# Optimization experiments

Hardware: AMD Instinct MI355X
Metric: run time of the kernel (lower is better)

## Reference

```python
import jax, jax.numpy as jnp
import numpy as np

B, N, E = 64, 512, 262144
D_EMB = 128   # 2 * embedding_dim
D_H = 128     # residue_emb_dim == iegmn_lay_hid_dim
L = 5         # iegmn_n_lays
X_INIT = 0.25 # residual mix toward original coords (IEGMN x_connection_init)


def silu(x):
    return x * jax.nn.sigmoid(x)


def _edges(k):
    # within-graph random edges: pick a graph, then a node inside it
    g = jax.random.randint(k, (E,), 0, B)
    n = jax.random.randint(jax.random.fold_in(k, 1), (E,), 0, N)
    return (g * N + n).astype(jnp.int32)


def setup_inputs() -> dict:
    key = jax.random.key(0)
    ks = jax.random.split(key, 16)
    Nt = B * N
    s = 0.05
    feat = jax.random.normal(ks[0], (Nt, D_EMB), jnp.float32)
    coords = jax.random.normal(ks[1], (Nt, 3), jnp.float32)
    c_valid = (jax.random.uniform(ks[2], (B, N)) > 0.3).astype(jnp.float32)
    c_valid = c_valid.at[:, 0].set(1.0)  # avoid empty graphs
    return {
        'feat': feat,
        'coords': coords,
        'c_valid': c_valid,
        'edge_src': _edges(ks[3]), 'edge_dst': _edges(ks[4]),
        'cross_src': _edges(ks[5]), 'cross_dst': _edges(ks[6]),
        'W_emb': jax.random.normal(ks[7], (D_H, D_EMB), jnp.float32) * s,
        'We1': jax.random.normal(ks[8], (L, 2 * D_H + 1, D_H), jnp.float32) * s,
        'be1': jnp.zeros((L, D_H), jnp.float32),
        'We2': jax.random.normal(ks[9], (L, D_H, D_H), jnp.float32) * s,
        'be2': jnp.zeros((L, D_H), jnp.float32),
        'Wx': jax.random.normal(ks[10], (L, D_H, 1), jnp.float32) * s,
        'Wh': jax.random.normal(ks[11], (L, 3 * D_H, D_H), jnp.float32) * s,
        'bh': jnp.zeros((L, D_H), jnp.float32),
        'Wfc': jax.random.normal(ks[12], (3, D_H, D_H), jnp.float32) * s,
        'bfc': jnp.zeros((3, D_H), jnp.float32),
        'Wout': jax.random.normal(ks[13], (D_H, 1), jnp.float32) * s,
        'bout': jnp.zeros((1,), jnp.float32),
    }


def _deg_inv(dst, n):
    deg = jax.ops.segment_sum(jnp.ones(dst.shape[0], jnp.float32), dst, num_segments=n)
    return (1.0 / jnp.maximum(deg, 1.0))[:, None]


def _iegmn_layer(p, src, dst, x, h, x0, h0, deg_inv):
    We1, be1, We2, be2, Wx, Wh, bh = p
    n = x.shape[0]
    dx = x[src] - x[dst]                                  # [E, 3]
    d2 = jnp.sum(dx * dx, -1, keepdims=True)              # [E, 1]
    m = silu(jnp.concatenate([h[src], h[dst], d2], -1) @ We1 + be1)
    m = silu(m @ We2 + be2)                               # [E, D_H]
    coef = jnp.tanh(m @ Wx)                               # [E, 1]
    agg_x = jax.ops.segment_sum(dx * coef, dst, num_segments=n) * deg_inv
    x_new = X_INIT * x0 + (1.0 - X_INIT) * x + agg_x
    agg_m = jax.ops.segment_sum(m, dst, num_segments=n) * deg_inv
    h_new = silu(jnp.concatenate([h, agg_m, h0], -1) @ Wh + bh)
    return x_new, h_new


def reference(feat, coords, c_valid, edge_src, edge_dst, cross_src, cross_dst,
              W_emb, We1, be1, We2, be2, Wx, Wh, bh, Wfc, bfc, Wout, bout):
    Nt = feat.shape[0]
    h = feat @ W_emb.T          # embede (no bias)
    h0, x0, x = h, coords, coords
    dgi = _deg_inv(edge_dst, Nt)
    dci = _deg_inv(cross_dst, Nt)
    for k in range(L):
        p = tuple(t[k] for t in (We1, be1, We2, be2, Wx, Wh, bh))
        # branch == 'both': run layer on graph then cross_graph with same input h
        x, c1 = _iegmn_layer(p, edge_src, edge_dst, x, h, x0, h0, dgi)
        x, c2 = _iegmn_layer(p, cross_src, cross_dst, x, h, x0, h0, dci)
        h = c2 - c1             # dropout is identity at inference
    # masked sum-pool / count
    hb = h.reshape(B, N, D_H)
    pooled = jnp.sum(hb * c_valid[..., None], axis=1) / jnp.sum(c_valid, axis=1, keepdims=True)
    z = pooled
    for i in range(Wfc.shape[0]):
        z = jax.nn.relu(z @ Wfc[i] + bfc[i])
    out = jax.nn.sigmoid(z @ Wout + bout)
    return out.reshape(-1)      # [B]
```

## Files before the change

kernel.cpp:

```cpp
#include <hip/hip_runtime.h>

#define DEVINL __device__ __forceinline__

constexpr int NT   = 32768;
constexpr int DH   = 128;
constexpr int NE   = 262144;
constexpr int BGR  = 64;
constexpr int NPG  = 512;
constexpr int LAYS = 5;

typedef __attribute__((ext_vector_type(8))) short bf16x8;
typedef __attribute__((ext_vector_type(4))) float f32x4;
typedef __attribute__((ext_vector_type(4))) unsigned int uint4v;
typedef unsigned int uint;

DEVINL float siluf(float v){ return v * (1.0f/(1.0f + __expf(-v))); }
DEVINL float tanh_fast(float x){ float e = __expf(2.0f*x); return 1.0f - 2.0f/(e + 1.0f); }

DEVINL uint bf16_rne(float f){
  uint x = __float_as_uint(f);
  return (x + 0x7fffu + ((x>>16)&1u)) >> 16;
}

DEVINL void split8(const float* m, bf16x8& h, bf16x8& l){
  #pragma unroll
  for (int j=0;j<8;j++){
    uint x  = __float_as_uint(m[j]);
    uint hb = x >> 16;
    float hf = __uint_as_float(hb<<16);
    uint lb = bf16_rne(m[j] - hf);
    h[j] = (short)hb; l[j] = (short)lb;
  }
}

DEVINL f32x4 mma3(bf16x8 ah, bf16x8 al, bf16x8 bh, bf16x8 bl, f32x4 acc){
  acc = __builtin_amdgcn_mfma_f32_16x16x32_bf16(al, bh, acc, 0,0,0);
  acc = __builtin_amdgcn_mfma_f32_16x16x32_bf16(ah, bl, acc, 0,0,0);
  acc = __builtin_amdgcn_mfma_f32_16x16x32_bf16(ah, bh, acc, 0,0,0);
  return acc;
}

template<int TRANS>
__global__ __launch_bounds__(256) void k_prep(const float* __restrict__ src, short* __restrict__ dst){
  const int idx = blockIdx.x*256 + threadIdx.x;
  const int k = idx>>7, col = idx&127;
  const float v = TRANS ? src[(size_t)col*128 + k] : src[(size_t)k*128 + col];
  uint hb = __float_as_uint(v) >> 16;
  float hf = __uint_as_float(hb<<16);
  uint lb = bf16_rne(v - hf);
  const int kc = k>>5, q = (k&31)>>3, j = k&7;
  const size_t o = (size_t)kc*8192 + q*1024 + col*8 + j;
  dst[o]        = (short)hb;
  dst[o + 4096] = (short)lb;
}

__global__ __launch_bounds__(256) void k_hist(const int* __restrict__ dst, int* __restrict__ cnt){
  int e = blockIdx.x*256 + threadIdx.x;
  atomicAdd(&cnt[dst[e]], 1);
}

__global__ __launch_bounds__(1024) void k_scan(const int* __restrict__ cnt, int* __restrict__ cur){
  __shared__ int part[1024];
  const int tid = threadIdx.x;
  const int base = tid*32;
  int s = 0;
  for (int i=0;i<32;i++) s += cnt[base+i];
  const int own = s;
  part[tid] = s; __syncthreads();
  for (int off=1; off<1024; off<<=1){
    int v = (tid>=off) ? part[tid-off] : 0;
    __syncthreads();
    part[tid] += v;
    __syncthreads();
  }
  int run = part[tid] - own;
  for (int i=0;i<32;i++){ cur[base+i] = run; run += cnt[base+i]; }
}

__global__ __launch_bounds__(256) void k_invdeg(const int* __restrict__ cnt, float* __restrict__ dinv){
  int n = blockIdx.x*256 + threadIdx.x;
  int c = cnt[n];
  dinv[n] = 1.0f / (float)(c > 1 ? c : 1);
}

__global__ __launch_bounds__(256) void k_scatter(const int* __restrict__ dst, int* __restrict__ cur,
                                                 int* __restrict__ perm){
  int e = blockIdx.x*256 + threadIdx.x;
  int p = atomicAdd(&cur[dst[e]], 1);
  perm[p] = e;
}

template<int MODE>
__global__ __launch_bounds__(512) void k_ngemm(
    const float* __restrict__ A0, float* __restrict__ A1, const float* __restrict__ A2,
    const float* __restrict__ dinv, const short* __restrict__ W0, const short* __restrict__ W1,
    const float* __restrict__ bias, const float* __restrict__ c1in,
    float* __restrict__ out0, float* __restrict__ out1)
{
  __shared__ __align__(16) short wbuf[16384];
  const int tid = threadIdx.x;
  const int wv = tid>>6, lane = tid&63, c = lane&15, q = lane>>4;
  const int row = blockIdx.x*128 + wv*16 + c;
  float dv = 1.0f;
  if constexpr (MODE>=2) dv = dinv[row];
  f32x4 accA[8], accB[8];
  #pragma unroll
  for (int t=0;t<8;t++){
    #pragma unroll
    for (int r=0;r<4;r++){ accA[t][r]=0.f; if constexpr (MODE==1) accB[t][r]=0.f; }
  }
  const int fo = q*1024 + c*8;
  constexpr int NST = (MODE==1) ? 4 : ((MODE>=2) ? 6 : 2);
  for (int st=0; st<NST; ++st){
    __syncthreads();
    if constexpr (MODE==1){
      #pragma unroll
      for (int i=0;i<2;i++){
        ((uint4v*)wbuf)[tid + i*512]         = ((const uint4v*)(W0 + st*8192))[tid + i*512];
        ((uint4v*)(wbuf+8192))[tid + i*512]  = ((const uint4v*)(W1 + st*8192))[tid + i*512];
      }
    } else {
      #pragma unroll
      for (int i=0;i<4;i++)
        ((uint4v*)wbuf)[tid + i*512] = ((const uint4v*)(W0 + (size_t)st*16384))[tid + i*512];
    }
    __syncthreads();
    if constexpr (MODE==1){
      const int kb = st*32 + q*8;
      float4 v0 = *(const float4*)(A0 + (size_t)row*128 + kb);
      float4 v1 = *(const float4*)(A0 + (size_t)row*128 + kb + 4);
      float m[8] = {v0.x,v0.y,v0.z,v0.w,v1.x,v1.y,v1.z,v1.w};
      bf16x8 ah, al; split8(m, ah, al);
      #pragma unroll
      for (int t=0;t<8;t++){
        bf16x8 bhA = *(const bf16x8*)&wbuf[t*128 + fo];
        bf16x8 blA = *(const bf16x8*)&wbuf[4096 + t*128 + fo];
        bf16x8 bhB = *(const bf16x8*)&wbuf[8192 + t*128 + fo];
        bf16x8 blB = *(const bf16x8*)&wbuf[12288 + t*128 + fo];
        accA[t] = mma3(ah, al, bhA, blA, accA[t]);
        accB[t] = mma3(ah, al, bhB, blB, accB[t]);
      }
    } else {
      #pragma unroll
      for (int ks=0; ks<2; ++ks){
        const int kc = st*2 + ks;
        const float* asrc = A0; float sc = 1.0f; bool zero_a1 = false;
        if constexpr (MODE>=2){
          if (kc >= 8)      { asrc = A2; }
          else if (kc >= 4) { asrc = A1; sc = dv; zero_a1 = true; }
        }
        const int koff = (kc&3)*32 + q*8;
        float4 v0 = *(const float4*)(asrc + (size_t)row*128 + koff);
        float4 v1 = *(const float4*)(asrc + (size_t)row*128 + koff + 4);
        if constexpr (MODE>=2){
          if (zero_a1){
            float4 z; z.x=0.f; z.y=0.f; z.z=0.f; z.w=0.f;
            *(float4*)(A1 + (size_t)row*128 + koff)     = z;
            *(float4*)(A1 + (size_t)row*128 + koff + 4) = z;
          }
        }
        float m[8] = {v0.x*sc,v0.y*sc,v0.z*sc,v0.w*sc,v1.x*sc,v1.y*sc,v1.z*sc,v1.w*sc};
        bf16x8 ah, al; split8(m, ah, al);
        #pragma unroll
        for (int t=0;t<8;t++){
          bf16x8 bh = *(const bf16x8*)&wbuf[ks*8192 + t*128 + fo];
          bf16x8 bl = *(const bf16x8*)&wbuf[ks*8192 + 4096 + t*128 + fo];
          accA[t] = mma3(ah, al, bh, bl, accA[t]);
        }
      }
    }
  }
  #pragma unroll
  for (int t=0;t<8;t++){
    const int col = t*16 + c;
    float b0 = 0.f;
    if constexpr (MODE!=0) b0 = bias[col];
    #pragma unroll
    for (int r=0;r<4;r++){
      const size_t orow = (size_t)blockIdx.x*128 + wv*16 + q*4 + r;
      float v = accA[t][r];
      if constexpr (MODE==0){
        out0[orow*128 + col] = v; out1[orow*128 + col] = v;
      } else if constexpr (MODE==1){
        out0[orow*128 + col] = v + b0;
        out1[orow*128 + col] = accB[t][r];
      } else if constexpr (MODE==2){
        out0[orow*128 + col] = siluf(v + b0);
      } else {
        out0[orow*128 + col] = siluf(v + b0) - c1in[orow*128 + col];
      }
    }
  }
}

__global__ __launch_bounds__(512) void k_edge(
    const int* __restrict__ perm, const int* __restrict__ esrc, const int* __restrict__ edst,
    const float* __restrict__ x,  const float* __restrict__ Aw, const float* __restrict__ Bw,
    const short* __restrict__ w2p, const float* __restrict__ We1_l,
    const float* __restrict__ be2_l, const float* __restrict__ Wx_l,
    float* __restrict__ aggm, float* __restrict__ aggx)
{
  __shared__ __align__(16) short w2t[16384];
  __shared__ __align__(16) float w256s[128];
  __shared__ __align__(16) float wxs[128];
  __shared__ __align__(16) float be2s[128];
  __shared__ float dxs[8][16][3];
  __shared__ int   dsts[8][16];
  const int tid = threadIdx.x;
  const int wv = tid>>6, lane = tid&63, c = lane&15, q = lane>>4;
  if (tid < 128){ w256s[tid]=We1_l[256*128+tid]; wxs[tid]=Wx_l[tid]; be2s[tid]=be2_l[tid]; }
  const int er = wv*16 + c;
  const int eg = perm[blockIdx.x*128 + er];
  const int s  = esrc[eg], d = edst[eg];
  const float dx0 = x[s*3+0]-x[d*3+0];
  const float dx1 = x[s*3+1]-x[d*3+1];
  const float dx2 = x[s*3+2]-x[d*3+2];
  const float d2  = dx0*dx0 + dx1*dx1 + dx2*dx2;
  if (q==0){ dxs[wv][c][0]=dx0; dxs[wv][c][1]=dx1; dxs[wv][c][2]=dx2; dsts[wv][c]=d; }
  f32x4 acc[8];
  #pragma unroll
  for (int t=0;t<8;t++){ acc[t][0]=0.f; acc[t][1]=0.f; acc[t][2]=0.f; acc[t][3]=0.f; }
  const int fo = q*1024 + c*8;
  const float* ap = Aw + (size_t)s*128;
  const float* bp = Bw + (size_t)d*128;
  for (int half=0; half<2; ++half){
    __syncthreads();
    #pragma unroll
    for (int i=0;i<4;i++)
      ((uint4v*)w2t)[tid + i*512] = ((const uint4v*)(w2p + half*16384))[tid + i*512];
    __syncthreads();
    #pragma unroll
    for (int ks=0; ks<2; ++ks){
      const int kb = half*64 + ks*32 + q*8;
      float4 av0 = *(const float4*)(ap+kb), av1 = *(const float4*)(ap+kb+4);
      float4 bv0 = *(const float4*)(bp+kb), bv1 = *(const float4*)(bp+kb+4);
      float4 w0  = *(const float4*)&w256s[kb], w1 = *(const float4*)&w256s[kb+4];
      float m[8];
      m[0]=siluf(av0.x+bv0.x+d2*w0.x); m[1]=siluf(av0.y+bv0.y+d2*w0.y);
      m[2]=siluf(av0.z+bv0.z+d2*w0.z); m[3]=siluf(av0.w+bv0.w+d2*w0.w);
      m[4]=siluf(av1.x+bv1.x+d2*w1.x); m[5]=siluf(av1.y+bv1.y+d2*w1.y);
      m[6]=siluf(av1.z+bv1.z+d2*w1.z); m[7]=siluf(av1.w+bv1.w+d2*w1.w);
      bf16x8 ah, al; split8(m, ah, al);
      #pragma unroll
      for (int t=0;t<8;t++){
        bf16x8 bh = *(const bf16x8*)&w2t[ks*8192 + t*128 + fo];
        bf16x8 bl = *(const bf16x8*)&w2t[ks*8192 + 4096 + t*128 + fo];
        acc[t] = mma3(ah, al, bh, bl, acc[t]);
      }
    }
  }
  float pd[4];
  #pragma unroll
  for (int t=0;t<8;t++){
    const float be = be2s[t*16+c], wx = wxs[t*16+c];
    #pragma unroll
    for (int r=0;r<4;r++){
      float v = siluf(acc[t][r] + be);
      acc[t][r] = v;
      if (t==0) pd[r] = v*wx; else pd[r] += v*wx;
    }
  }
  #pragma unroll
  for (int msk=1; msk<16; msk<<=1){
    #pragma unroll
    for (int r=0;r<4;r++) pd[r] += __shfl_xor(pd[r], msk);
  }
  const int rb = q*4;
  const int rd0 = dsts[wv][rb+0], rd1 = dsts[wv][rb+1];
  const int rd2 = dsts[wv][rb+2], rd3 = dsts[wv][rb+3];
  const bool b1 = (rd1!=rd0), b2 = (rd2!=rd1), b3 = (rd3!=rd2);
  {
    #pragma unroll
    for (int t=0;t<8;t++){
      const int col = t*16 + c;
      float v3 = acc[t][3];
      float v2 = acc[t][2] + (b3 ? 0.f : v3);
      float v1 = acc[t][1] + (b2 ? 0.f : v2);
      float v0 = acc[t][0] + (b1 ? 0.f : v1);
      unsafeAtomicAdd(aggm + (size_t)rd0*128 + col, v0);
      if (b1) unsafeAtomicAdd(aggm + (size_t)rd1*128 + col, v1);
      if (b2) unsafeAtomicAdd(aggm + (size_t)rd2*128 + col, v2);
      if (b3) unsafeAtomicAdd(aggm + (size_t)rd3*128 + col, v3);
    }
  }
  if (c < 3){
    float a0 = dxs[wv][rb+0][c]*tanh_fast(pd[0]);
    float a1 = dxs[wv][rb+1][c]*tanh_fast(pd[1]);
    float a2 = dxs[wv][rb+2][c]*tanh_fast(pd[2]);
    float a3 = dxs[wv][rb+3][c]*tanh_fast(pd[3]);
    float v3 = a3;
    float v2 = a2 + (b3 ? 0.f : v3);
    float v1 = a1 + (b2 ? 0.f : v2);
    float v0 = a0 + (b1 ? 0.f : v1);
    unsafeAtomicAdd(aggx + (size_t)rd0*3 + c, v0);
    if (b1) unsafeAtomicAdd(aggx + (size_t)rd1*3 + c, v1);
    if (b2) unsafeAtomicAdd(aggx + (size_t)rd2*3 + c, v2);
    if (b3) unsafeAtomicAdd(aggx + (size_t)rd3*3 + c, v3);
  }
}

__global__ __launch_bounds__(256) void k_xupd(float* __restrict__ x, const float* __restrict__ x0,
                                              float* __restrict__ aggx,
                                              const float* __restrict__ dinv){
  int i = blockIdx.x*256 + threadIdx.x;
  if (i < NT*3){
    int n = i/3;
    x[i] = 0.25f*x0[i] + 0.75f*x[i] + aggx[i]*dinv[n];
    aggx[i] = 0.f;
  }
}

__global__ __launch_bounds__(512) void k_pool(const float* __restrict__ h,
                                              const float* __restrict__ cvalid,
                                              float* __restrict__ pooled){
  __shared__ float red[4][128];
  __shared__ float redc[4];
  const int b = blockIdx.x, t = threadIdx.x, j = t&127, sl = t>>7;
  float s = 0.f, cf = 0.f;
  for (int n=sl; n<NPG; n+=4){
    const float m = cvalid[b*NPG + n];
    s  += h[((size_t)b*NPG + n)*DH + j] * m;
    cf += m;
  }
  red[sl][j] = s;
  if (j==0) redc[sl] = cf;
  __syncthreads();
  if (t < 128){
    float ss = red[0][t]+red[1][t]+red[2][t]+red[3][t];
    float cc = redc[0]+redc[1]+redc[2]+redc[3];
    pooled[b*DH + t] = ss / cc;
  }
}

__global__ __launch_bounds__(256) void k_mlp(const float* __restrict__ pooled,
                                             const float* __restrict__ Wfc,
                                             const float* __restrict__ bfc,
                                             const float* __restrict__ Wout,
                                             const float* __restrict__ bout,
                                             float* __restrict__ out)
{
  __shared__ __align__(16) float z[64*132];
  __shared__ __align__(16) float wB[128*128];
  const int t = threadIdx.x;
  {
    const int n = t>>2, qq = t&3;
    const float4* p = (const float4*)(pooled + n*DH + qq*32);
    float4* w = (float4*)&z[n*132 + qq*32];
    #pragma unroll
    for (int u=0;u<8;u++) w[u] = p[u];
  }
  const int g = t>>5, lane = t&31, c0 = lane*4;
  for (int l=0;l<3;l++){
    #pragma unroll
    for (int i=0;i<16;i++){
      const int idx = t + i*256;
      ((float4*)wB)[idx] = ((const float4*)(Wfc + (size_t)l*DH*DH))[idx];
    }
    __syncthreads();
    float acc[8][4];
    #pragma unroll
    for (int i=0;i<8;i++){ acc[i][0]=0.f; acc[i][1]=0.f; acc[i][2]=0.f; acc[i][3]=0.f; }
    #pragma unroll 4
    for (int kk=0; kk<128; kk+=4){
      float4 b0=*(const float4*)&wB[(kk+0)*128+c0];
      float4 b1=*(const float4*)&wB[(kk+1)*128+c0];
      float4 b2=*(const float4*)&wB[(kk+2)*128+c0];
      float4 b3=*(const float4*)&wB[(kk+3)*128+c0];
      #pragma unroll
      for (int i=0;i<8;i++){
        float4 a=*(const float4*)&z[(g*8+i)*132 + kk];
        acc[i][0]+=a.x*b0.x+a.y*b1.x+a.z*b2.x+a.w*b3.x;
        acc[i][1]+=a.x*b0.y+a.y*b1.y+a.z*b2.y+a.w*b3.y;
        acc[i][2]+=a.x*b0.z+a.y*b1.z+a.z*b2.z+a.w*b3.z;
        acc[i][3]+=a.x*b0.w+a.y*b1.w+a.z*b2.w+a.w*b3.w;
      }
    }
    __syncthreads();
    #pragma unroll
    for (int i=0;i<8;i++){
      float v0=acc[i][0]+bfc[l*DH+c0+0]; v0 = v0>0.f?v0:0.f;
      float v1=acc[i][1]+bfc[l*DH+c0+1]; v1 = v1>0.f?v1:0.f;
      float v2=acc[i][2]+bfc[l*DH+c0+2]; v2 = v2>0.f?v2:0.f;
      float v3=acc[i][3]+bfc[l*DH+c0+3]; v3 = v3>0.f?v3:0.f;
      float4 v; v.x=v0; v.y=v1; v.z=v2; v.w=v3;
      *(float4*)&z[(g*8+i)*132 + c0] = v;
    }
    __syncthreads();
  }
  if (t < 64){
    float a = 0.f;
    for (int k2=0;k2<128;k2++) a += z[t*132 + k2]*Wout[k2];
    out[t] = 1.0f/(1.0f + __expf(-(a + bout[0])));
  }
}

extern "C" void kernel_launch(void* const* d_in, const int* in_sizes, int n_in,
                              void* d_out, int out_size, void* d_ws, size_t ws_size,
                              hipStream_t stream)
{
  (void)in_sizes; (void)n_in; (void)out_size; (void)ws_size;
  const float* feat   = (const float*)d_in[0];
  const float* coords = (const float*)d_in[1];
  const float* cvalid = (const float*)d_in[2];
  const int*   esrc   = (const int*)d_in[3];
  const int*   edst   = (const int*)d_in[4];
  const int*   csrc   = (const int*)d_in[5];
  const int*   cdst   = (const int*)d_in[6];
  const float* W_emb  = (const float*)d_in[7];
  const float* We1    = (const float*)d_in[8];
  const float* be1    = (const float*)d_in[9];
  const float* We2    = (const float*)d_in[10];
  const float* be2    = (const float*)d_in[11];
  const float* Wx     = (const float*)d_in[12];
  const float* Wh     = (const float*)d_in[13];
  const float* bh     = (const float*)d_in[14];
  const float* Wfc    = (const float*)d_in[15];
  const float* bfc    = (const float*)d_in[16];
  const float* Wout   = (const float*)d_in[17];
  const float* bout   = (const float*)d_in[18];

  float* ws = (float*)d_ws;
  float* h      = ws; ws += (size_t)NT*DH;
  float* h0     = ws; ws += (size_t)NT*DH;
  float* c1     = ws; ws += (size_t)NT*DH;
  float* Aw     = ws; ws += (size_t)NT*DH;
  float* Bw     = ws; ws += (size_t)NT*DH;
  float* aggm   = ws; ws += (size_t)NT*DH;
  float* x      = ws; ws += (size_t)NT*3;
  float* aggx   = ws; ws += (size_t)NT*3;
  float* dgi    = ws; ws += NT;
  float* dci    = ws; ws += NT;
  float* pooled = ws; ws += BGR*DH;
  int* permG  = (int*)ws; ws += NE;
  int* permC  = (int*)ws; ws += NE;
  int* cnt    = (int*)ws; ws += NT;
  int* cursor = (int*)ws; ws += NT;
  short* pst    = (short*)ws;
  short* wemb_p = pst;
  const size_t LSTR = 32768*3 + 98304;
  short* lay_p  = pst + 32768;

  hipMemsetAsync(aggm, 0, (size_t)NT*DH*sizeof(float), stream);
  hipMemsetAsync(aggx, 0, (size_t)NT*3*sizeof(float), stream);

  k_prep<1><<<64, 256, 0, stream>>>(W_emb, wemb_p);
  for (int k=0;k<LAYS;k++){
    short* p = lay_p + (size_t)k*LSTR;
    k_prep<0><<<64,  256, 0, stream>>>(We1 + (size_t)k*257*DH,          p);
    k_prep<0><<<64,  256, 0, stream>>>(We1 + (size_t)k*257*DH + 128*DH, p + 32768);
    k_prep<0><<<64,  256, 0, stream>>>(We2 + (size_t)k*DH*DH,           p + 65536);
    k_prep<0><<<192, 256, 0, stream>>>(Wh  + (size_t)k*3*DH*DH,         p + 98304);
  }

  hipMemsetAsync(cnt, 0, NT*sizeof(int), stream);
  k_hist   <<<NE/256, 256, 0, stream>>>(edst, cnt);
  k_scan   <<<1, 1024, 0, stream>>>(cnt, cursor);
  k_invdeg <<<NT/256, 256, 0, stream>>>(cnt, dgi);
  k_scatter<<<NE/256, 256, 0, stream>>>(edst, cursor, permG);
  hipMemsetAsync(cnt, 0, NT*sizeof(int), stream);
  k_hist   <<<NE/256, 256, 0, stream>>>(cdst, cnt);
  k_scan   <<<1, 1024, 0, stream>>>(cnt, cursor);
  k_invdeg <<<NT/256, 256, 0, stream>>>(cnt, dci);
  k_scatter<<<NE/256, 256, 0, stream>>>(cdst, cursor, permC);

  k_ngemm<0><<<NT/128, 512, 0, stream>>>(feat, nullptr, nullptr, nullptr,
                                         wemb_p, nullptr, nullptr, nullptr, h, h0);
  hipMemcpyAsync(x, coords, (size_t)NT*3*sizeof(float), hipMemcpyDeviceToDevice, stream);

  for (int k=0; k<LAYS; k++){
    short* p = lay_p + (size_t)k*LSTR;
    const float* We1_l = We1 + (size_t)k*257*DH;
    const float* be1_l = be1 + (size_t)k*DH;
    const float* be2_l = be2 + (size_t)k*DH;
    const float* Wx_l  = Wx  + (size_t)k*DH;
    const float* bh_l  = bh  + (size_t)k*DH;

    k_ngemm<1><<<NT/128, 512, 0, stream>>>(h, nullptr, nullptr, nullptr,
                                           p, p + 32768, be1_l, nullptr, Aw, Bw);
    k_edge<<<NE/128, 512, 0, stream>>>(permG, esrc, edst, x, Aw, Bw,
                                       p + 65536, We1_l, be2_l, Wx_l, aggm, aggx);
    k_xupd<<<(NT*3+255)/256, 256, 0, stream>>>(x, coords, aggx, dgi);
    k_ngemm<2><<<NT/128, 512, 0, stream>>>(h, aggm, h0, dgi,
                                           p + 98304, nullptr, bh_l, nullptr, c1, nullptr);
    k_edge<<<NE/128, 512, 0, stream>>>(permC, csrc, cdst, x, Aw, Bw,
                                       p + 65536, We1_l, be2_l, Wx_l, aggm, aggx);
    k_xupd<<<(NT*3+255)/256, 256, 0, stream>>>(x, coords, aggx, dci);
    k_ngemm<3><<<NT/128, 512, 0, stream>>>(h, aggm, h0, dci,
                                           p + 98304, nullptr, bh_l, c1, h, nullptr);
  }

  k_pool<<<BGR, 512, 0, stream>>>(h, cvalid, pooled);
  k_mlp <<<1, 256, 0, stream>>>(pooled, Wfc, bfc, Wout, bout, (float*)d_out);
}
```

Baseline: 1.694 ms.

## Merge preprocessing launches and restructure node GEMM to read weights directly

Folds the 21 weight-prep launches into one kernel and merges the edge-sort pipeline for both graphs into paired hist/scan/scatter kernels, folding the inverse-degree computation into the scan. The node GEMM drops its LDS weight staging and per-stage barriers. Blocks now cover 64 rows with the 8 waves split across output-column halves, reading bf16 weights straight from global/L2. The aggm zeroing moves to the end of the GEMM behind a barrier. The tradeoff is more global weight reads per block and twice as many blocks, in exchange for fewer launches and no LDS synchronization.

```diff
diff --git a/kernel.cpp b/kernel.cpp
--- a/kernel.cpp
+++ b/kernel.cpp
@@ -8,6 +8,7 @@
 constexpr int BGR  = 64;
 constexpr int NPG  = 512;
 constexpr int LAYS = 5;
+constexpr size_t LSTR = 32768*3 + 98304;
 
 typedef __attribute__((ext_vector_type(8))) short bf16x8;
 typedef __attribute__((ext_vector_type(4))) float f32x4;
@@ -40,54 +41,78 @@
   return acc;
 }
 
-template<int TRANS>
-__global__ __launch_bounds__(256) void k_prep(const float* __restrict__ src, short* __restrict__ dst){
+__global__ __launch_bounds__(256) void k_prep_all(
+    const float* __restrict__ W_emb, const float* __restrict__ We1,
+    const float* __restrict__ We2,  const float* __restrict__ Wh,
+    short* __restrict__ wemb_p, short* __restrict__ lay_p)
+{
   const int idx = blockIdx.x*256 + threadIdx.x;
-  const int k = idx>>7, col = idx&127;
-  const float v = TRANS ? src[(size_t)col*128 + k] : src[(size_t)k*128 + col];
-  uint hb = __float_as_uint(v) >> 16;
+  const float* src; short* dst; int v; bool trans = false;
+  if (idx < 16384){ src = W_emb; dst = wemb_p; v = idx; trans = true; }
+  else {
+    const int u = idx - 16384;
+    const int layer = u / 98304;
+    const int w = u - layer*98304;
+    short* p = lay_p + (size_t)layer*LSTR;
+    if (w < 16384)      { src = We1 + (size_t)layer*257*DH;          dst = p;         v = w; }
+    else if (w < 32768) { src = We1 + (size_t)layer*257*DH + 128*DH; dst = p + 32768; v = w - 16384; }
+    else if (w < 49152) { src = We2 + (size_t)layer*DH*DH;           dst = p + 65536; v = w - 32768; }
+    else                { src = Wh  + (size_t)layer*3*DH*DH;         dst = p + 98304; v = w - 49152; }
+  }
+  const int k = v>>7, col = v&127;
+  const float val = trans ? src[(size_t)col*128 + k] : src[(size_t)k*128 + col];
+  uint hb = __float_as_uint(val) >> 16;
   float hf = __uint_as_float(hb<<16);
-  uint lb = bf16_rne(v - hf);
+  uint lb = bf16_rne(val - hf);
   const int kc = k>>5, q = (k&31)>>3, j = k&7;
   const size_t o = (size_t)kc*8192 + q*1024 + col*8 + j;
   dst[o]        = (short)hb;
   dst[o + 4096] = (short)lb;
 }
 
-__global__ __launch_bounds__(256) void k_hist(const int* __restrict__ dst, int* __restrict__ cnt){
-  int e = blockIdx.x*256 + threadIdx.x;
-  atomicAdd(&cnt[dst[e]], 1);
-}
-
-__global__ __launch_bounds__(1024) void k_scan(const int* __restrict__ cnt, int* __restrict__ cur){
+__global__ __launch_bounds__(256) void k_hist2(const int* __restrict__ edst,
+                                               const int* __restrict__ cdst,
+                                               int* __restrict__ cnt){
+  const int half = blockIdx.x >= (NE/256);
+  const int e = (blockIdx.x - half*(NE/256))*256 + threadIdx.x;
+  const int* d = half ? cdst : edst;
+  atomicAdd(&cnt[half*NT + d[e]], 1);
+}
+
+__global__ __launch_bounds__(1024) void k_scan2(const int* __restrict__ cnt,
+                                                int* __restrict__ cur,
+                                                float* __restrict__ dinv){
   __shared__ int part[1024];
+  const int off = blockIdx.x * NT;
   const int tid = threadIdx.x;
   const int base = tid*32;
   int s = 0;
-  for (int i=0;i<32;i++) s += cnt[base+i];
+  for (int i=0;i<32;i++){
+    const int c = cnt[off + base + i];
+    dinv[off + base + i] = 1.0f / (float)(c > 1 ? c : 1);
+    s += c;
+  }
   const int own = s;
   part[tid] = s; __syncthreads();
-  for (int off=1; off<1024; off<<=1){
-    int v = (tid>=off) ? part[tid-off] : 0;
+  for (int o=1; o<1024; o<<=1){
+    int v = (tid>=o) ? part[tid-o] : 0;
     __syncthreads();
     part[tid] += v;
     __syncthreads();
   }
   int run = part[tid] - own;
-  for (int i=0;i<32;i++){ cur[base+i] = run; run += cnt[base+i]; }
-}
-
-__global__ __launch_bounds__(256) void k_invdeg(const int* __restrict__ cnt, float* __restrict__ dinv){
-  int n = blockIdx.x*256 + threadIdx.x;
-  int c = cnt[n];
-  dinv[n] = 1.0f / (float)(c > 1 ? c : 1);
-}
-
-__global__ __launch_bounds__(256) void k_scatter(const int* __restrict__ dst, int* __restrict__ cur,
-                                                 int* __restrict__ perm){
-  int e = blockIdx.x*256 + threadIdx.x;
-  int p = atomicAdd(&cur[dst[e]], 1);
-  perm[p] = e;
+  for (int i=0;i<32;i++){ cur[off + base + i] = run; run += cnt[off + base + i]; }
+}
+
+__global__ __launch_bounds__(256) void k_scatter2(const int* __restrict__ edst,
+                                                  const int* __restrict__ cdst,
+                                                  int* __restrict__ cur,
+                                                  int* __restrict__ perm){
+  const int half = blockIdx.x >= (NE/256);
+  const int e = (blockIdx.x - half*(NE/256))*256 + threadIdx.x;
+  const int* d = half ? cdst : edst;
+  const int p = atomicAdd(&cur[half*NT + d[e]], 1);
+  perm[half*NE + p] = e;
 }
 
 template<int MODE>
@@ -97,99 +122,70 @@
     const float* __restrict__ bias, const float* __restrict__ c1in,
     float* __restrict__ out0, float* __restrict__ out1)
 {
-  __shared__ __align__(16) short wbuf[16384];
   const int tid = threadIdx.x;
   const int wv = tid>>6, lane = tid&63, c = lane&15, q = lane>>4;
-  const int row = blockIdx.x*128 + wv*16 + c;
+  const int rowt = wv & 3, grp = wv >> 2;
+  const int row = blockIdx.x*64 + rowt*16 + c;
+  constexpr int KC = (MODE>=2) ? 12 : 4;
+  constexpr int TT = (MODE==1) ? 8 : 4;
   float dv = 1.0f;
   if constexpr (MODE>=2) dv = dinv[row];
-  f32x4 accA[8], accB[8];
-  #pragma unroll
-  for (int t=0;t<8;t++){
-    #pragma unroll
-    for (int r=0;r<4;r++){ accA[t][r]=0.f; if constexpr (MODE==1) accB[t][r]=0.f; }
-  }
-  const int fo = q*1024 + c*8;
-  constexpr int NST = (MODE==1) ? 4 : ((MODE>=2) ? 6 : 2);
-  for (int st=0; st<NST; ++st){
-    __syncthreads();
-    if constexpr (MODE==1){
-      #pragma unroll
-      for (int i=0;i<2;i++){
-        ((uint4v*)wbuf)[tid + i*512]         = ((const uint4v*)(W0 + st*8192))[tid + i*512];
-        ((uint4v*)(wbuf+8192))[tid + i*512]  = ((const uint4v*)(W1 + st*8192))[tid + i*512];
-      }
-    } else {
-      #pragma unroll
-      for (int i=0;i<4;i++)
-        ((uint4v*)wbuf)[tid + i*512] = ((const uint4v*)(W0 + (size_t)st*16384))[tid + i*512];
-    }
-    __syncthreads();
-    if constexpr (MODE==1){
-      const int kb = st*32 + q*8;
-      float4 v0 = *(const float4*)(A0 + (size_t)row*128 + kb);
-      float4 v1 = *(const float4*)(A0 + (size_t)row*128 + kb + 4);
-      float m[8] = {v0.x,v0.y,v0.z,v0.w,v1.x,v1.y,v1.z,v1.w};
-      bf16x8 ah, al; split8(m, ah, al);
-      #pragma unroll
-      for (int t=0;t<8;t++){
-        bf16x8 bhA = *(const bf16x8*)&wbuf[t*128 + fo];
-        bf16x8 blA = *(const bf16x8*)&wbuf[4096 + t*128 + fo];
-        bf16x8 bhB = *(const bf16x8*)&wbuf[8192 + t*128 + fo];
-        bf16x8 blB = *(const bf16x8*)&wbuf[12288 + t*128 + fo];
-        accA[t] = mma3(ah, al, bhA, blA, accA[t]);
-        accB[t] = mma3(ah, al, bhB, blB, accB[t]);
-      }
-    } else {
-      #pragma unroll
-      for (int ks=0; ks<2; ++ks){
-        const int kc = st*2 + ks;
-        const float* asrc = A0; float sc = 1.0f; bool zero_a1 = false;
-        if constexpr (MODE>=2){
-          if (kc >= 8)      { asrc = A2; }
-          else if (kc >= 4) { asrc = A1; sc = dv; zero_a1 = true; }
-        }
-        const int koff = (kc&3)*32 + q*8;
-        float4 v0 = *(const float4*)(asrc + (size_t)row*128 + koff);
-        float4 v1 = *(const float4*)(asrc + (size_t)row*128 + koff + 4);
-        if constexpr (MODE>=2){
-          if (zero_a1){
-            float4 z; z.x=0.f; z.y=0.f; z.z=0.f; z.w=0.f;
-            *(float4*)(A1 + (size_t)row*128 + koff)     = z;
-            *(float4*)(A1 + (size_t)row*128 + koff + 4) = z;
-          }
-        }
-        float m[8] = {v0.x*sc,v0.y*sc,v0.z*sc,v0.w*sc,v1.x*sc,v1.y*sc,v1.z*sc,v1.w*sc};
-        bf16x8 ah, al; split8(m, ah, al);
-        #pragma unroll
-        for (int t=0;t<8;t++){
-          bf16x8 bh = *(const bf16x8*)&wbuf[ks*8192 + t*128 + fo];
-          bf16x8 bl = *(const bf16x8*)&wbuf[ks*8192 + 4096 + t*128 + fo];
-          accA[t] = mma3(ah, al, bh, bl, accA[t]);
-        }
-      }
-    }
-  }
-  #pragma unroll
-  for (int t=0;t<8;t++){
-    const int col = t*16 + c;
+  const short* Wp = W0;
+  if constexpr (MODE==1){ if (grp==1) Wp = W1; }
+  f32x4 acc[TT];
+  #pragma unroll
+  for (int t=0;t<TT;t++){ acc[t][0]=0.f; acc[t][1]=0.f; acc[t][2]=0.f; acc[t][3]=0.f; }
+
+  #pragma unroll
+  for (int kc=0; kc<KC; ++kc){
+    const float* asrc = A0; float sc = 1.0f;
+    if constexpr (MODE>=2){
+      if (kc >= 8)      { asrc = A2; }
+      else if (kc >= 4) { asrc = A1; sc = dv; }
+    }
+    const int koff = (kc&3)*32 + q*8;
+    float4 v0 = *(const float4*)(asrc + (size_t)row*128 + koff);
+    float4 v1 = *(const float4*)(asrc + (size_t)row*128 + koff + 4);
+    float m[8] = {v0.x*sc,v0.y*sc,v0.z*sc,v0.w*sc,v1.x*sc,v1.y*sc,v1.z*sc,v1.w*sc};
+    bf16x8 ah, al; split8(m, ah, al);
+    #pragma unroll
+    for (int t=0;t<TT;t++){
+      const int tg = (MODE==1) ? t : grp*4 + t;
+      const short* fp = Wp + (size_t)kc*8192 + q*1024 + (tg*16 + c)*8;
+      bf16x8 bh = *(const bf16x8*)fp;
+      bf16x8 bl = *(const bf16x8*)(fp + 4096);
+      acc[t] = mma3(ah, al, bh, bl, acc[t]);
+    }
+  }
+  #pragma unroll
+  for (int t=0;t<TT;t++){
+    const int tg = (MODE==1) ? t : grp*4 + t;
+    const int col = tg*16 + c;
     float b0 = 0.f;
-    if constexpr (MODE!=0) b0 = bias[col];
+    if constexpr (MODE==1){ if (grp==0) b0 = bias[col]; }
+    else if constexpr (MODE>=2){ b0 = bias[col]; }
     #pragma unroll
     for (int r=0;r<4;r++){
-      const size_t orow = (size_t)blockIdx.x*128 + wv*16 + q*4 + r;
-      float v = accA[t][r];
+      const size_t orow = (size_t)blockIdx.x*64 + rowt*16 + q*4 + r;
+      float v = acc[t][r];
       if constexpr (MODE==0){
         out0[orow*128 + col] = v; out1[orow*128 + col] = v;
       } else if constexpr (MODE==1){
-        out0[orow*128 + col] = v + b0;
-        out1[orow*128 + col] = accB[t][r];
+        if (grp==0) out0[orow*128 + col] = v + b0;
+        else        out1[orow*128 + col] = v;
       } else if constexpr (MODE==2){
         out0[orow*128 + col] = siluf(v + b0);
       } else {
         out0[orow*128 + col] = siluf(v + b0) - c1in[orow*128 + col];
       }
     }
+  }
+  if constexpr (MODE>=2){
+    __syncthreads();
+    float4 z; z.x=0.f; z.y=0.f; z.z=0.f; z.w=0.f;
+    float4* zp = (float4*)(A1 + (size_t)blockIdx.x*64*128);
+    #pragma unroll
+    for (int i=0;i<4;i++) zp[tid + i*512] = z;
   }
 }
 
@@ -426,45 +422,30 @@
   float* Aw     = ws; ws += (size_t)NT*DH;
   float* Bw     = ws; ws += (size_t)NT*DH;
   float* aggm   = ws; ws += (size_t)NT*DH;
+  float* aggx   = ws; ws += (size_t)NT*3;
   float* x      = ws; ws += (size_t)NT*3;
-  float* aggx   = ws; ws += (size_t)NT*3;
   float* dgi    = ws; ws += NT;
   float* dci    = ws; ws += NT;
   float* pooled = ws; ws += BGR*DH;
   int* permG  = (int*)ws; ws += NE;
   int* permC  = (int*)ws; ws += NE;
-  int* cnt    = (int*)ws; ws += NT;
-  int* cursor = (int*)ws; ws += NT;
+  int* cnt    = (int*)c1;
+  int* cursor = cnt + 2*NT;
   short* pst    = (short*)ws;
   short* wemb_p = pst;
-  const size_t LSTR = 32768*3 + 98304;
   short* lay_p  = pst + 32768;
 
-  hipMemsetAsync(aggm, 0, (size_t)NT*DH*sizeof(float), stream);
-  hipMemsetAsync(aggx, 0, (size_t)NT*3*sizeof(float), stream);
-
-  k_prep<1><<<64, 256, 0, stream>>>(W_emb, wemb_p);
-  for (int k=0;k<LAYS;k++){
-    short* p = lay_p + (size_t)k*LSTR;
-    k_prep<0><<<64,  256, 0, stream>>>(We1 + (size_t)k*257*DH,          p);
-    k_prep<0><<<64,  256, 0, stream>>>(We1 + (size_t)k*257*DH + 128*DH, p + 32768);
-    k_prep<0><<<64,  256, 0, stream>>>(We2 + (size_t)k*DH*DH,           p + 65536);
-    k_prep<0><<<192, 256, 0, stream>>>(Wh  + (size_t)k*3*DH*DH,         p + 98304);
-  }
-
-  hipMemsetAsync(cnt, 0, NT*sizeof(int), stream);
-  k_hist   <<<NE/256, 256, 0, stream>>>(edst, cnt);
-  k_scan   <<<1, 1024, 0, stream>>>(cnt, cursor);
-  k_invdeg <<<NT/256, 256, 0, stream>>>(cnt, dgi);
-  k_scatter<<<NE/256, 256, 0, stream>>>(edst, cursor, permG);
-  hipMemsetAsync(cnt, 0, NT*sizeof(int), stream);
-  k_hist   <<<NE/256, 256, 0, stream>>>(cdst, cnt);
-  k_scan   <<<1, 1024, 0, stream>>>(cnt, cursor);
-  k_invdeg <<<NT/256, 256, 0, stream>>>(cnt, dci);
-  k_scatter<<<NE/256, 256, 0, stream>>>(cdst, cursor, permC);
-
-  k_ngemm<0><<<NT/128, 512, 0, stream>>>(feat, nullptr, nullptr, nullptr,
-                                         wemb_p, nullptr, nullptr, nullptr, h, h0);
+  hipMemsetAsync(aggm, 0, (size_t)NT*(DH+3)*sizeof(float), stream);
+
+  k_prep_all<<<1984, 256, 0, stream>>>(W_emb, We1, We2, Wh, wemb_p, lay_p);
+
+  hipMemsetAsync(cnt, 0, 2*NT*sizeof(int), stream);
+  k_hist2   <<<2*(NE/256), 256, 0, stream>>>(edst, cdst, cnt);
+  k_scan2   <<<2, 1024, 0, stream>>>(cnt, cursor, dgi);
+  k_scatter2<<<2*(NE/256), 256, 0, stream>>>(edst, cdst, cursor, permG);
+
+  k_ngemm<0><<<NT/64, 512, 0, stream>>>(feat, nullptr, nullptr, nullptr,
+                                        wemb_p, nullptr, nullptr, nullptr, h, h0);
   hipMemcpyAsync(x, coords, (size_t)NT*3*sizeof(float), hipMemcpyDeviceToDevice, stream);
 
   for (int k=0; k<LAYS; k++){
@@ -475,18 +456,18 @@
     const float* Wx_l  = Wx  + (size_t)k*DH;
     const float* bh_l  = bh  + (size_t)k*DH;
 
-    k_ngemm<1><<<NT/128, 512, 0, stream>>>(h, nullptr, nullptr, nullptr,
-                                           p, p + 32768, be1_l, nullptr, Aw, Bw);
+    k_ngemm<1><<<NT/64, 512, 0, stream>>>(h, nullptr, nullptr, nullptr,
+                                          p, p + 32768, be1_l, nullptr, Aw, Bw);
     k_edge<<<NE/128, 512, 0, stream>>>(permG, esrc, edst, x, Aw, Bw,
                                        p + 65536, We1_l, be2_l, Wx_l, aggm, aggx);
     k_xupd<<<(NT*3+255)/256, 256, 0, stream>>>(x, coords, aggx, dgi);
-    k_ngemm<2><<<NT/128, 512, 0, stream>>>(h, aggm, h0, dgi,
-                                           p + 98304, nullptr, bh_l, nullptr, c1, nullptr);
-    k_edge<<<NE/128, 512, 0, stream>>>(permC, csrc, cdst, x, Aw, Bw,
+    k_ngemm<2><<<NT/64, 512, 0, stream>>>(h, aggm, h0, dgi,
+                                          p + 98304, nullptr, bh_l, nullptr, c1, nullptr);
+    k_edge<<<NE/128, 512, 0, stream>>>(permG + NE, csrc, cdst, x, Aw, Bw,
                                        p + 65536, We1_l, be2_l, Wx_l, aggm, aggx);
     k_xupd<<<(NT*3+255)/256, 256, 0, stream>>>(x, coords, aggx, dci);
-    k_ngemm<3><<<NT/128, 512, 0, stream>>>(h, aggm, h0, dci,
-                                           p + 98304, nullptr, bh_l, c1, h, nullptr);
+    k_ngemm<3><<<NT/64, 512, 0, stream>>>(h, aggm, h0, dci,
+                                          p + 98304, nullptr, bh_l, c1, h, nullptr);
   }
 
   k_pool<<<BGR, 512, 0, stream>>>(h, cvalid, pooled);
```

Result: slower. 1.780 ms (+5.0%).
